# Performance work log

Measured on AMD Instinct MI355X. Metric: run time of the kernel, lower is better.

The kernel has to match this reference:

```python
import jax, jax.numpy as jnp
import numpy as np

N_NODES = 100000
N_EDGES = 1600000
N_GRAPHS = 256
HIDDEN = 128
IN_FEAT = 5


def setup_inputs() -> dict:
    key = jax.random.key(0)
    ks = jax.random.split(key, 12)
    x = jax.random.normal(ks[0], (N_NODES, IN_FEAT), dtype=jnp.float32)
    edge_index = jax.random.randint(ks[1], (2, N_EDGES), 0, N_NODES, dtype=jnp.int64)
    batch = jnp.sort(jax.random.randint(ks[2], (N_NODES,), 0, N_GRAPHS, dtype=jnp.int64))
    s = 0.05
    W0 = jax.random.normal(ks[3], (IN_FEAT, HIDDEN), dtype=jnp.float32) * s
    b0 = jnp.zeros((HIDDEN,), dtype=jnp.float32)
    W1 = jax.random.normal(ks[4], (HIDDEN, HIDDEN), dtype=jnp.float32) * s
    b1 = jnp.zeros((HIDDEN,), dtype=jnp.float32)
    W2 = jax.random.normal(ks[5], (HIDDEN, HIDDEN), dtype=jnp.float32) * s
    b2 = jnp.zeros((HIDDEN,), dtype=jnp.float32)
    lin_w = jax.random.normal(ks[6], (HIDDEN, 1), dtype=jnp.float32) * s
    lin_b = jnp.zeros((1,), dtype=jnp.float32)
    return {"x": x, "edge_index": edge_index, "batch": batch,
            "W0": W0, "b0": b0, "W1": W1, "b1": b1, "W2": W2, "b2": b2,
            "lin_w": lin_w, "lin_b": lin_b}


def reference(x, edge_index, batch, W0, b0, W1, b1, W2, b2, lin_w, lin_b):
    n = x.shape[0]
    # PyG GCNConv: add self-loops, symmetric normalization D^-1/2 (A+I) D^-1/2
    loop = jnp.arange(n, dtype=edge_index.dtype)
    src = jnp.concatenate([edge_index[0], loop])  # [E+N]
    dst = jnp.concatenate([edge_index[1], loop])
    deg = jax.ops.segment_sum(jnp.ones_like(dst, dtype=x.dtype), dst, num_segments=n)
    dis = jnp.where(deg > 0, jax.lax.rsqrt(jnp.maximum(deg, 1.0)), 0.0)
    norm = (dis[src] * dis[dst])[:, None]  # [E+N, 1]

    def gcn_conv(h, W, b):
        h = h @ W                      # [N, H]
        msg = h[src] * norm            # gather + scale, [E+N, H]
        return jax.ops.segment_sum(msg, dst, num_segments=n) + b

    h = jax.nn.relu(gcn_conv(x, W0, b0))
    h = jax.nn.relu(gcn_conv(h, W1, b1))
    h = gcn_conv(h, W2, b2)

    # global_mean_pool over batch ids
    sums = jax.ops.segment_sum(h, batch, num_segments=N_GRAPHS)
    cnt = jax.ops.segment_sum(jnp.ones((n,), x.dtype), batch, num_segments=N_GRAPHS)
    g = sums / jnp.maximum(cnt, 1.0)[:, None]
    # dropout p=0.01 is identity in eval mode
    return jax.nn.sigmoid(g @ lin_w + lin_b)  # [N_GRAPHS, 1]
```

## Files before the change

kernel.cpp:

```cpp
#include <hip/hip_runtime.h>

#define GCN_N 100000
#define GCN_H 128
#define GCN_G 256
#define NPB_SHIFT 9
#define NPB 512
#define NBKT 196
#define CHUNK 2048
#define SRC_BITS 17
#define SRC_MASK ((1 << SRC_BITS) - 1)
#define EBUF_CAP 10240

static_assert(GCN_N < (1 << SRC_BITS), "src id must fit 17 bits");

using short8 = __attribute__((ext_vector_type(8))) short;
using f32x4  = __attribute__((ext_vector_type(4))) float;
using f32x2  = __attribute__((ext_vector_type(2))) float;

#if defined(__has_builtin)
#if __has_builtin(__builtin_amdgcn_cvt_scalef32_pk_f32_fp4)
#define HW_FP4 1
#endif
#endif


__device__ __forceinline__ unsigned short f2bf(float f) {
    unsigned u = __float_as_uint(f);
    unsigned r = u + 0x7FFFu + ((u >> 16) & 1u);
    return (unsigned short)(r >> 16);
}
__device__ __forceinline__ float bf2f(unsigned short h) {
    return __uint_as_float(((unsigned)h) << 16);
}

__device__ __forceinline__ void fp4x8_to_f32(unsigned v, float* f) {
#ifdef HW_FP4
    f32x2 p0 = __builtin_amdgcn_cvt_scalef32_pk_f32_fp4(v, 1.0f, 0);
    f32x2 p1 = __builtin_amdgcn_cvt_scalef32_pk_f32_fp4(v, 1.0f, 1);
    f32x2 p2 = __builtin_amdgcn_cvt_scalef32_pk_f32_fp4(v, 1.0f, 2);
    f32x2 p3 = __builtin_amdgcn_cvt_scalef32_pk_f32_fp4(v, 1.0f, 3);
    f[0] = p0[0]; f[1] = p0[1]; f[2] = p1[0]; f[3] = p1[1];
    f[4] = p2[0]; f[5] = p2[1]; f[6] = p3[0]; f[7] = p3[1];
#else
    #pragma unroll
    for (int j = 0; j < 8; j++) {
        unsigned nib = (v >> (4 * j)) & 0xF;
        unsigned e = (nib >> 1) & 3, m = nib & 1;
        float mag = (e == 0) ? 0.5f * (float)m : ldexpf(1.0f + 0.5f * (float)m, (int)e - 1);
        f[j] = (nib & 8) ? -mag : mag;
    }
#endif
}

__device__ __forceinline__ unsigned f32_to_fp4(float a) {
    unsigned sg = (a < 0.f) ? 8u : 0u;
    float b = fabsf(a);
    unsigned q = (unsigned)(b >= 0.25f) + (unsigned)(b >= 0.75f) + (unsigned)(b >= 1.25f)
               + (unsigned)(b >= 1.75f) + (unsigned)(b >= 2.5f) + (unsigned)(b >= 3.5f)
               + (unsigned)(b >= 5.0f);
    return sg | q;
}


__global__ __launch_bounds__(256) void hist_prep_kernel(const int* __restrict__ dst,
                                                        int* __restrict__ hist, int E, int B,
                                                        const float* __restrict__ W1,
                                                        const float* __restrict__ W2,
                                                        const float* __restrict__ b2,
                                                        const float* __restrict__ lw,
                                                        unsigned short* __restrict__ w1t,
                                                        float* __restrict__ w2l,
                                                        float* __restrict__ c2) {
    __shared__ int lh[NBKT];
    __shared__ float slw[128];
    int blk = blockIdx.x, tid = threadIdx.x;
    if (blk < B) {
        if (tid < NBKT) lh[tid] = 0;
        __syncthreads();
        int e0 = blk * CHUNK;
        #pragma unroll
        for (int i = 0; i < CHUNK / 256; i++) {
            int e = e0 + tid + i * 256;
            if (e < E) atomicAdd(&lh[dst[e] >> NPB_SHIFT], 1);
        }
        __syncthreads();
        if (tid < NBKT) hist[(size_t)blk * NBKT + tid] = lh[tid];
    } else if (blk < B + 64) {
        int idx = (blk - B) * 256 + tid;
        int col = idx >> 7, k = idx & 127;
        w1t[idx] = f2bf(W1[k * 128 + col]);
    } else {
        if (tid < 128) slw[tid] = lw[tid];
        __syncthreads();
        if (tid < 128) {
            float s = 0.f;
            #pragma unroll 8
            for (int j = 0; j < 128; j++) s = fmaf(W2[tid * 128 + j], slw[j], s);
            w2l[tid] = s;
        } else if (tid == 128) {
            float s = 0.f;
            for (int j = 0; j < 128; j++) s = fmaf(b2[j], slw[j], s);
            c2[0] = s;
        }
    }
}

__global__ __launch_bounds__(64) void scan_cols_kernel(const int* __restrict__ hist,
                                                       int* __restrict__ offsT,
                                                       int* __restrict__ btot, int B) {
    int k = blockIdx.x;
    int lane = threadIdx.x;
    int running = 0;
    for (int b0 = 0; b0 < B; b0 += 64) {
        int b = b0 + lane;
        int v = (b < B) ? hist[(size_t)b * NBKT + k] : 0;
        int iv = v;
        #pragma unroll
        for (int d = 1; d < 64; d <<= 1) {
            int x = __shfl_up(iv, d, 64);
            if (lane >= d) iv += x;
        }
        if (b < B) offsT[(size_t)k * B + b] = running + iv - v;
        running += __shfl(iv, 63, 64);
    }
    if (lane == 0) btot[k] = running;
}

__global__ __launch_bounds__(256) void partition_kernel(const int* __restrict__ src,
                                                        const int* __restrict__ dst,
                                                        const int* __restrict__ btot,
                                                        const int* __restrict__ offsT,
                                                        int* __restrict__ epack,
                                                        int E, int B) {
    __shared__ int cur[NBKT];
    __shared__ int sbase[NBKT];
    int blk = blockIdx.x, tid = threadIdx.x;
    if (tid == 0) {
        int run = 0;
        for (int kk = 0; kk < NBKT; kk++) { sbase[kk] = run; run += btot[kk]; }
    }
    __syncthreads();
    if (tid < NBKT) cur[tid] = sbase[tid] + offsT[(size_t)tid * B + blk];
    __syncthreads();
    int e0 = blk * CHUNK;
    #pragma unroll
    for (int i = 0; i < CHUNK / 256; i++) {
        int e = e0 + tid + i * 256;
        if (e < E) {
            int d = dst[e];
            int s = src[e];
            int pos = atomicAdd(&cur[d >> NPB_SHIFT], 1);
            epack[pos] = ((d & (NPB - 1)) << SRC_BITS) | s;
        }
    }
}

__global__ __launch_bounds__(512) void csr_build_kernel(const int* __restrict__ epack,
                                                        const int* __restrict__ btot,
                                                        const float* __restrict__ x,
                                                        int* __restrict__ rowptr,
                                                        float* __restrict__ dis,
                                                        float* __restrict__ xsp,
                                                        int* __restrict__ csrc, int n) {
    __shared__ int ebuf[EBUF_CAP];
    __shared__ int lcount[NPB];
    __shared__ int lcur[NPB];
    __shared__ int wsums[8];
    __shared__ int s_eb, s_ee, s_tot;
    int k = blockIdx.x, tid = threadIdx.x;
    int lane = tid & 63, wid = tid >> 6;
    int nodebase = k << NPB_SHIFT;

    lcount[tid] = 0;
    if (tid == 0) {
        int run = 0, eb = 0, ee = 0;
        for (int kk = 0; kk < NBKT; kk++) {
            if (kk == k) eb = run;
            run += btot[kk];
            if (kk == k) ee = run;
        }
        s_eb = eb; s_ee = ee; s_tot = run;
    }
    __syncthreads();
    int ebeg = s_eb, eend = s_ee;
    bool fits = (eend - ebeg) <= EBUF_CAP;

    for (int e = ebeg + tid; e < eend; e += 512) {
        int p = epack[e];
        if (fits) ebuf[e - ebeg] = p;
        atomicAdd(&lcount[p >> SRC_BITS], 1);
    }
    __syncthreads();

    int v = lcount[tid];
    int iv = v;
    #pragma unroll
    for (int d = 1; d < 64; d <<= 1) {
        int x2 = __shfl_up(iv, d, 64);
        if (lane >= d) iv += x2;
    }
    if (lane == 63) wsums[wid] = iv;
    __syncthreads();
    if (tid == 0) {
        int r = 0;
        #pragma unroll
        for (int w = 0; w < 8; w++) { int t = wsums[w]; wsums[w] = r; r += t; }
    }
    __syncthreads();
    int ex = wsums[wid] + iv - v;
    lcur[tid] = ex;
    int node = nodebase + tid;
    if (node < n) {
        rowptr[node] = ebeg + ex;
        float dd = rsqrtf((float)(v + 1));
        dis[node] = dd;
        const float* xr = x + (size_t)node * 5;
        float4 a;
        a.x = xr[0] * dd; a.y = xr[1] * dd; a.z = xr[2] * dd; a.w = xr[3] * dd;
        float a4 = xr[4] * dd;
        ((float4*)(xsp + (size_t)node * 8))[0] = a;
        xsp[(size_t)node * 8 + 4] = a4;
        xsp[(size_t)node * 8 + 5] = 0.f;
        xsp[(size_t)node * 8 + 6] = 0.f;
        xsp[(size_t)node * 8 + 7] = 0.f;
    }
    if (k == NBKT - 1 && tid == 0) rowptr[n] = s_tot;
    __syncthreads();
    for (int e = ebeg + tid; e < eend; e += 512) {
        int p = fits ? ebuf[e - ebeg] : epack[e];
        int pos = atomicAdd(&lcur[p >> SRC_BITS], 1);
        csrc[ebeg + pos] = p & SRC_MASK;
    }
}


__global__ __launch_bounds__(256) void mmfused_kernel(const float* __restrict__ xsp,
                                                      const int* __restrict__ rowptr,
                                                      const int* __restrict__ csrc,
                                                      const float* __restrict__ W0,
                                                      const float* __restrict__ b0,
                                                      const unsigned short* __restrict__ w1t,
                                                      const float* __restrict__ dis,
                                                      unsigned* __restrict__ t1q4,
                                                      float* __restrict__ tscale, int n) {
    __shared__ __align__(16) unsigned short sA[128 * 128];
    __shared__ __align__(16) unsigned short sBT[128 * 128];
    __shared__ __align__(16) float sA0f[128 * 8];
    __shared__ float sDis[128];
    __shared__ float sSmax[128];
    char* sAb = (char*)sA;
    char* sBb = (char*)sBT;
    int tid = threadIdx.x;
    int rowBase = blockIdx.x * 128;

    if (tid < 128) {
        int i = rowBase + tid;
        float a[5] = {0.f, 0.f, 0.f, 0.f, 0.f};
        float di = 0.f;
        if (i < n) {
            di = dis[i];
            const float* xr = xsp + (size_t)i * 8;
            float4 s4 = ((const float4*)xr)[0];
            a[0] = s4.x; a[1] = s4.y; a[2] = s4.z; a[3] = s4.w; a[4] = xr[4];
            int r0 = rowptr[i], r1 = rowptr[i + 1];
            int e = r0;
            for (; e + 7 < r1; e += 8) {
                int ss[8];
                #pragma unroll
                for (int u = 0; u < 8; u++) ss[u] = csrc[e + u];
                float4 v[8]; float a4[8];
                #pragma unroll
                for (int u = 0; u < 8; u++) {
                    v[u] = ((const float4*)(xsp + (size_t)ss[u] * 8))[0];
                    a4[u] = xsp[(size_t)ss[u] * 8 + 4];
                }
                #pragma unroll
                for (int u = 0; u < 8; u++) {
                    a[0] += v[u].x; a[1] += v[u].y; a[2] += v[u].z; a[3] += v[u].w;
                    a[4] += a4[u];
                }
            }
            for (; e < r1; e++) {
                int s = csrc[e];
                float4 v = ((const float4*)(xsp + (size_t)s * 8))[0];
                a[0] += v.x; a[1] += v.y; a[2] += v.z; a[3] += v.w;
                a[4] += xsp[(size_t)s * 8 + 4];
            }
            #pragma unroll
            for (int j = 0; j < 5; j++) a[j] *= di;
        }
        sDis[tid] = di;
        #pragma unroll
        for (int j = 0; j < 5; j++) sA0f[tid * 8 + j] = a[j];
    } else {
        int t2 = tid - 128;
        #pragma unroll
        for (int it = 0; it < 16; it++) {
            int idx = t2 + it * 128;
            int col = idx >> 4, c = idx & 15;
            uint4 v = ((const uint4*)w1t)[idx];
            int byteoff = (col * 256 + c * 16) ^ ((col & 7) << 4);
            *(uint4*)(sBb + byteoff) = v;
        }
    }
    __syncthreads();

    {
        int cq = tid & 31;
        int rg = tid >> 5;
        float4 w0q[5];
        #pragma unroll
        for (int j = 0; j < 5; j++) w0q[j] = *((const float4*)(W0 + j * 128 + cq * 4));
        float4 b0q = *((const float4*)(b0 + cq * 4));
        #pragma unroll
        for (int ri = 0; ri < 16; ri++) {
            int row = rg + ri * 8;
            const float* ar = sA0f + row * 8;
            float4 h = b0q;
            #pragma unroll
            for (int j = 0; j < 5; j++) {
                float aj = ar[j];
                h.x = fmaf(aj, w0q[j].x, h.x);
                h.y = fmaf(aj, w0q[j].y, h.y);
                h.z = fmaf(aj, w0q[j].z, h.z);
                h.w = fmaf(aj, w0q[j].w, h.w);
            }
            h.x = fmaxf(h.x, 0.f); h.y = fmaxf(h.y, 0.f);
            h.z = fmaxf(h.z, 0.f); h.w = fmaxf(h.w, 0.f);
            uint2 p;
            p.x = (unsigned)f2bf(h.x) | ((unsigned)f2bf(h.y) << 16);
            p.y = (unsigned)f2bf(h.z) | ((unsigned)f2bf(h.w) << 16);
            int byteoff = (row * 256 + cq * 8) ^ ((row & 7) << 4);
            *(uint2*)(sAb + byteoff) = p;
        }
    }
    __syncthreads();

    int wave = tid >> 6, l = tid & 63;
    int lr = l & 15, lg = l >> 4;
    int rb = wave * 32;

    short8 afr[2][4];
    #pragma unroll
    for (int rt = 0; rt < 2; rt++) {
        int row = rb + rt * 16 + lr;
        #pragma unroll
        for (int ks = 0; ks < 4; ks++) {
            int byteoff = (row * 256 + ks * 64 + lg * 16) ^ ((row & 7) << 4);
            afr[rt][ks] = *(const short8*)(sAb + byteoff);
        }
    }
    f32x4 acc[2][8];
    #pragma unroll
    for (int rt = 0; rt < 2; rt++)
        #pragma unroll
        for (int ct = 0; ct < 8; ct++)
            acc[rt][ct] = (f32x4){0.f, 0.f, 0.f, 0.f};

    #pragma unroll
    for (int ct = 0; ct < 8; ct++) {
        int col = ct * 16 + lr;
        short8 bfr[4];
        #pragma unroll
        for (int ks = 0; ks < 4; ks++) {
            int byteoff = (col * 256 + ks * 64 + lg * 16) ^ ((col & 7) << 4);
            bfr[ks] = *(const short8*)(sBb + byteoff);
        }
        #pragma unroll
        for (int rt = 0; rt < 2; rt++) {
            #pragma unroll
            for (int ks = 0; ks < 4; ks++) {
                acc[rt][ct] = __builtin_amdgcn_mfma_f32_16x16x32_bf16(
                    afr[rt][ks], bfr[ks], acc[rt][ct], 0, 0, 0);
            }
        }
    }

    #pragma unroll
    for (int rt = 0; rt < 2; rt++) {
        #pragma unroll
        for (int i = 0; i < 4; i++) {
            int rowL = rb + rt * 16 + lg * 4 + i;
            float dsc = sDis[rowL];
            float m = 0.f;
            #pragma unroll
            for (int ct = 0; ct < 8; ct++) {
                int col = ct * 16 + lr;
                float vv = acc[rt][ct][i] * dsc;
                int byteoff = (rowL * 256 + col * 2) ^ ((rowL & 7) << 4);
                *(unsigned short*)(sAb + byteoff) = f2bf(vv);
                m = fmaxf(m, fabsf(vv));
            }
            #pragma unroll
            for (int msk = 1; msk < 16; msk <<= 1)
                m = fmaxf(m, __shfl_xor(m, msk, 64));
            if (lr == 0) sSmax[rowL] = m;
        }
    }
    __syncthreads();

    #pragma unroll
    for (int it = 0; it < 8; it++) {
        int flat = tid + it * 256;
        int rowL = flat >> 4, c16 = flat & 15;
        int gr = rowBase + rowL;
        if (gr < n) {
            int byteoff = (rowL * 256 + c16 * 16) ^ ((rowL & 7) << 4);
            uint4 v = *(const uint4*)(sAb + byteoff);
            float ff[8];
            ff[0] = __uint_as_float(v.x << 16); ff[1] = __uint_as_float(v.x & 0xFFFF0000u);
            ff[2] = __uint_as_float(v.y << 16); ff[3] = __uint_as_float(v.y & 0xFFFF0000u);
            ff[4] = __uint_as_float(v.z << 16); ff[5] = __uint_as_float(v.z & 0xFFFF0000u);
            ff[6] = __uint_as_float(v.w << 16); ff[7] = __uint_as_float(v.w & 0xFFFF0000u);
            float s6 = sSmax[rowL] * (1.f / 6.f);
            float inv = (s6 > 0.f) ? 1.f / s6 : 0.f;
            unsigned q = 0;
            #pragma unroll
            for (int j = 0; j < 8; j++) q |= f32_to_fp4(ff[j] * inv) << (4 * j);
            t1q4[(size_t)gr * 16 + c16] = q;
            if (c16 == 0) tscale[gr] = s6;
        }
    }
}


__global__ __launch_bounds__(256) void agg1_kernel(const unsigned* __restrict__ t1q4,
                                                   const float* __restrict__ tscale,
                                                   const float* __restrict__ dis,
                                                   const int* __restrict__ rowptr,
                                                   const int* __restrict__ csrc,
                                                   const float* __restrict__ b1,
                                                   const float* __restrict__ w2l,
                                                   float* __restrict__ z, int n) {
    int group = threadIdx.x >> 4, lane = threadIdx.x & 15;
    int i = blockIdx.x * 16 + group;
    if (i >= n) return;
    float f[8], acc[8];
    unsigned sv = t1q4[(size_t)i * 16 + lane];
    float sci = tscale[i];
    fp4x8_to_f32(sv, f);
    #pragma unroll
    for (int j = 0; j < 8; j++) acc[j] = f[j] * sci;
    int r0 = rowptr[i], r1 = rowptr[i + 1];
    for (int e = r0; e < r1; e += 16) {
        int cnt = r1 - e; if (cnt > 16) cnt = 16;
        int idx = e + lane;
        int si = (idx < r1) ? csrc[idx] : 0;
        unsigned vv[16]; float sc[16];
        #pragma unroll
        for (int u = 0; u < 16; u++) {
            if (u < cnt) {
                int s = __shfl(si, u, 16);
                vv[u] = t1q4[(size_t)s * 16 + lane];
                sc[u] = tscale[s];
            }
        }
        #pragma unroll
        for (int u = 0; u < 16; u++) {
            if (u < cnt) {
                fp4x8_to_f32(vv[u], f);
                #pragma unroll
                for (int j = 0; j < 8; j++) acc[j] = fmaf(f[j], sc[u], acc[j]);
            }
        }
    }
    float di = dis[i];
    float4 b4a = ((const float4*)b1)[lane * 2];
    float4 b4b = ((const float4*)b1)[lane * 2 + 1];
    float4 w4a = ((const float4*)w2l)[lane * 2];
    float4 w4b = ((const float4*)w2l)[lane * 2 + 1];
    float bb[8] = {b4a.x, b4a.y, b4a.z, b4a.w, b4b.x, b4b.y, b4b.z, b4b.w};
    float ww[8] = {w4a.x, w4a.y, w4a.z, w4a.w, w4b.x, w4b.y, w4b.z, w4b.w};
    float d = 0.f;
    #pragma unroll
    for (int j = 0; j < 8; j++) {
        float c = fmaxf(fmaf(di, acc[j], bb[j]), 0.f);
        d = fmaf(c, ww[j], d);
    }
    #pragma unroll
    for (int o = 8; o > 0; o >>= 1) d += __shfl_down(d, o, 16);
    if (lane == 0) z[i] = di * d;
}


__global__ __launch_bounds__(256) void aggz_pool_kernel(const float* __restrict__ z,
                                                        const float* __restrict__ dis,
                                                        const int* __restrict__ rowptr,
                                                        const int* __restrict__ csrc,
                                                        const int* __restrict__ batch,
                                                        const float* __restrict__ c2,
                                                        const float* __restrict__ lb,
                                                        float* __restrict__ gsum,
                                                        int* __restrict__ gcnt,
                                                        int* __restrict__ done,
                                                        float* __restrict__ out, int n) {
    __shared__ float lg[GCN_G];
    __shared__ int lc[GCN_G];
    __shared__ int sticket;
    int tid = threadIdx.x;
    lg[tid] = 0.f;
    lc[tid] = 0;
    __syncthreads();
    int i = blockIdx.x * 256 + tid;
    bool valid = i < n;
    float ndv = 0.f;
    int g = 0;
    if (valid) {
        float acc = z[i];
        int r0 = rowptr[i], r1 = rowptr[i + 1];
        int e = r0;
        for (; e + 7 < r1; e += 8) {
            int ss[8];
            #pragma unroll
            for (int u = 0; u < 8; u++) ss[u] = csrc[e + u];
            float zv[8];
            #pragma unroll
            for (int u = 0; u < 8; u++) zv[u] = z[ss[u]];
            #pragma unroll
            for (int u = 0; u < 8; u++) acc += zv[u];
        }
        for (; e < r1; e++) acc += z[csrc[e]];
        ndv = dis[i] * acc;
        g = batch[i];
    }
    int lane = tid & 63;
    int g0 = __shfl(g, 0, 64);
    bool uni = __all(g == g0) && __all(valid);
    if (uni) {
        float s = ndv;
        #pragma unroll
        for (int o = 32; o > 0; o >>= 1) s += __shfl_down(s, o, 64);
        if (lane == 0) {
            atomicAdd(&lg[g0], s);
            atomicAdd(&lc[g0], 64);
        }
    } else if (valid) {
        atomicAdd(&lg[g], ndv);
        atomicAdd(&lc[g], 1);
    }
    __syncthreads();
    float v = lg[tid];
    int c = lc[tid];
    if (v != 0.f) atomicAdd(&gsum[tid], v);
    if (c != 0) atomicAdd(&gcnt[tid], c);

    __threadfence();
    if (tid == 0) sticket = atomicAdd(done, 1);
    __syncthreads();
    if (sticket == (int)gridDim.x - 1) {
        float sv = atomicAdd(&gsum[tid], 0.f);
        int cv = atomicAdd(&gcnt[tid], 0);
        float vv = sv / (float)max(cv, 1) + c2[0] + lb[0];
        out[tid] = 1.f / (1.f + expf(-vv));
    }
}


extern "C" void kernel_launch(void* const* d_in, const int* in_sizes, int n_in,
                              void* d_out, int out_size, void* d_ws, size_t ws_size,
                              hipStream_t stream) {
    const float* x   = (const float*)d_in[0];
    const int*   ei  = (const int*)d_in[1];
    const int*   bat = (const int*)d_in[2];
    const float* W0  = (const float*)d_in[3];
    const float* b0  = (const float*)d_in[4];
    const float* W1  = (const float*)d_in[5];
    const float* b1  = (const float*)d_in[6];
    const float* W2  = (const float*)d_in[7];
    const float* b2  = (const float*)d_in[8];
    const float* lw  = (const float*)d_in[9];
    const float* lb  = (const float*)d_in[10];
    float* out = (float*)d_out;

    const int N = GCN_N;
    const int E = in_sizes[1] / 2;
    const int B = (E + CHUNK - 1) / CHUNK;

    char* ws = (char*)d_ws;
    size_t off = 0;
    auto alloc = [&](size_t bytes) {
        size_t o = off;
        off += (bytes + 255) & ~(size_t)255;
        return o;
    };
    int*   hist    = (int*)(ws + alloc((size_t)B * NBKT * 4));
    int*   offsT   = (int*)(ws + alloc((size_t)NBKT * B * 4));
    int*   btot    = (int*)(ws + alloc((size_t)NBKT * 4));
    int*   epack   = (int*)(ws + alloc((size_t)E * 4));
    int*   rowptr  = (int*)(ws + alloc((size_t)(N + 1) * 4));
    float* dis     = (float*)(ws + alloc((size_t)N * 4));
    int*   csrc    = (int*)(ws + alloc((size_t)E * 4));
    float* xsp     = (float*)(ws + alloc((size_t)N * 8 * 4));
    unsigned* t1q4 = (unsigned*)(ws + alloc((size_t)N * 64));
    float* tscale  = (float*)(ws + alloc((size_t)N * 4));
    float* z       = (float*)(ws + alloc((size_t)N * 4));
    float* w2l     = (float*)(ws + alloc(128 * 4));
    float* c2      = (float*)(ws + alloc(4));
    unsigned short* w1t = (unsigned short*)(ws + alloc(128 * 128 * 2));
    float* gsum    = (float*)(ws + alloc(GCN_G * 4));
    int*   gcnt    = (int*)(ws + alloc(GCN_G * 4));
    int*   done    = (int*)(ws + alloc(4));

    const int* src = ei;
    const int* dst = ei + E;

    hipMemsetAsync(gsum, 0, GCN_G * 4 * 2 + 256, stream);

    hist_prep_kernel<<<B + 65, 256, 0, stream>>>(dst, hist, E, B, W1, W2, b2, lw, w1t, w2l, c2);
    scan_cols_kernel<<<NBKT, 64, 0, stream>>>(hist, offsT, btot, B);
    partition_kernel<<<B, 256, 0, stream>>>(src, dst, btot, offsT, epack, E, B);
    csr_build_kernel<<<NBKT, 512, 0, stream>>>(epack, btot, x, rowptr, dis, xsp, csrc, N);

    mmfused_kernel<<<(N + 127) / 128, 256, 0, stream>>>(xsp, rowptr, csrc, W0, b0, w1t, dis,
                                                        t1q4, tscale, N);
    agg1_kernel<<<(N + 15) / 16, 256, 0, stream>>>(t1q4, tscale, dis, rowptr, csrc, b1, w2l, z, N);
    aggz_pool_kernel<<<(N + 255) / 256, 256, 0, stream>>>(z, dis, rowptr, csrc, bat, c2, lb,
                                                          gsum, gcnt, done, out, N);
}
```

Baseline: 179.0 us.

## Split layer-0 neighbor aggregation into separate kernel before fused matmul

Moves the 5-feature neighbor gather for layer 0 out of the fused matmul kernel into a standalone aggx kernel that uses every thread, writing results to a new a0p buffer. The fused kernel then loads the aggregated rows and the W1 tile with all 256 threads instead of splitting the block half gather, half weight-load. This removes latency-bound, half-occupied gather work from the MFMA kernel at the cost of an extra launch and an extra global round trip of the aggregated features.

Result: slower. 183.2 us (+2.3%).

```diff
diff --git a/kernel.cpp b/kernel.cpp
--- a/kernel.cpp
+++ b/kernel.cpp
@@ -234,9 +234,47 @@
 }
 
 
-__global__ __launch_bounds__(256) void mmfused_kernel(const float* __restrict__ xsp,
-                                                      const int* __restrict__ rowptr,
-                                                      const int* __restrict__ csrc,
+__global__ __launch_bounds__(256) void aggx_kernel(const float* __restrict__ xsp,
+                                                   const float* __restrict__ dis,
+                                                   const int* __restrict__ rowptr,
+                                                   const int* __restrict__ csrc,
+                                                   float* __restrict__ a0p, int n) {
+    int i = blockIdx.x * 256 + threadIdx.x;
+    if (i >= n) return;
+    float4 acc = ((const float4*)(xsp + (size_t)i * 8))[0];
+    float acc4 = xsp[(size_t)i * 8 + 4];
+    int r0 = rowptr[i], r1 = rowptr[i + 1];
+    int e = r0;
+    for (; e + 7 < r1; e += 8) {
+        int ss[8];
+        #pragma unroll
+        for (int u = 0; u < 8; u++) ss[u] = csrc[e + u];
+        float4 v[8]; float a4[8];
+        #pragma unroll
+        for (int u = 0; u < 8; u++) {
+            v[u] = ((const float4*)(xsp + (size_t)ss[u] * 8))[0];
+            a4[u] = xsp[(size_t)ss[u] * 8 + 4];
+        }
+        #pragma unroll
+        for (int u = 0; u < 8; u++) {
+            acc.x += v[u].x; acc.y += v[u].y; acc.z += v[u].z; acc.w += v[u].w;
+            acc4 += a4[u];
+        }
+    }
+    for (; e < r1; e++) {
+        int s = csrc[e];
+        float4 v = ((const float4*)(xsp + (size_t)s * 8))[0];
+        acc.x += v.x; acc.y += v.y; acc.z += v.z; acc.w += v.w;
+        acc4 += xsp[(size_t)s * 8 + 4];
+    }
+    float di = dis[i];
+    acc.x *= di; acc.y *= di; acc.z *= di; acc.w *= di; acc4 *= di;
+    ((float4*)(a0p + (size_t)i * 8))[0] = acc;
+    a0p[(size_t)i * 8 + 4] = acc4;
+}
+
+
+__global__ __launch_bounds__(256) void mmfused_kernel(const float* __restrict__ a0p,
                                                       const float* __restrict__ W0,
                                                       const float* __restrict__ b0,
                                                       const unsigned short* __restrict__ w1t,
@@ -245,7 +283,7 @@
                                                       float* __restrict__ tscale, int n) {
     __shared__ __align__(16) unsigned short sA[128 * 128];
     __shared__ __align__(16) unsigned short sBT[128 * 128];
-    __shared__ __align__(16) float sA0f[128 * 8];
+    __shared__ __align__(16) float4 sA0[256];
     __shared__ float sDis[128];
     __shared__ float sSmax[128];
     char* sAb = (char*)sA;
@@ -253,55 +291,24 @@
     int tid = threadIdx.x;
     int rowBase = blockIdx.x * 128;
 
-    if (tid < 128) {
-        int i = rowBase + tid;
-        float a[5] = {0.f, 0.f, 0.f, 0.f, 0.f};
-        float di = 0.f;
-        if (i < n) {
-            di = dis[i];
-            const float* xr = xsp + (size_t)i * 8;
-            float4 s4 = ((const float4*)xr)[0];
-            a[0] = s4.x; a[1] = s4.y; a[2] = s4.z; a[3] = s4.w; a[4] = xr[4];
-            int r0 = rowptr[i], r1 = rowptr[i + 1];
-            int e = r0;
-            for (; e + 7 < r1; e += 8) {
-                int ss[8];
-                #pragma unroll
-                for (int u = 0; u < 8; u++) ss[u] = csrc[e + u];
-                float4 v[8]; float a4[8];
-                #pragma unroll
-                for (int u = 0; u < 8; u++) {
-                    v[u] = ((const float4*)(xsp + (size_t)ss[u] * 8))[0];
-                    a4[u] = xsp[(size_t)ss[u] * 8 + 4];
-                }
-                #pragma unroll
-                for (int u = 0; u < 8; u++) {
-                    a[0] += v[u].x; a[1] += v[u].y; a[2] += v[u].z; a[3] += v[u].w;
-                    a[4] += a4[u];
-                }
-            }
-            for (; e < r1; e++) {
-                int s = csrc[e];
-                float4 v = ((const float4*)(xsp + (size_t)s * 8))[0];
-                a[0] += v.x; a[1] += v.y; a[2] += v.z; a[3] += v.w;
-                a[4] += xsp[(size_t)s * 8 + 4];
-            }
-            #pragma unroll
-            for (int j = 0; j < 5; j++) a[j] *= di;
-        }
-        sDis[tid] = di;
-        #pragma unroll
-        for (int j = 0; j < 5; j++) sA0f[tid * 8 + j] = a[j];
-    } else {
-        int t2 = tid - 128;
-        #pragma unroll
-        for (int it = 0; it < 16; it++) {
-            int idx = t2 + it * 128;
-            int col = idx >> 4, c = idx & 15;
-            uint4 v = ((const uint4*)w1t)[idx];
-            int byteoff = (col * 256 + c * 16) ^ ((col & 7) << 4);
-            *(uint4*)(sBb + byteoff) = v;
-        }
+    {
+        int rowL = tid >> 1, q = tid & 1;
+        int gr = rowBase + rowL;
+        float4 v = make_float4(0.f, 0.f, 0.f, 0.f);
+        if (gr < n) v = ((const float4*)a0p)[(size_t)gr * 2 + q];
+        sA0[tid] = v;
+        if (tid < 128) {
+            int g2 = rowBase + tid;
+            sDis[tid] = (g2 < n) ? dis[g2] : 0.f;
+        }
+    }
+    #pragma unroll
+    for (int it = 0; it < 8; it++) {
+        int idx = tid + it * 256;
+        int col = idx >> 4, c = idx & 15;
+        uint4 v = ((const uint4*)w1t)[idx];
+        int byteoff = (col * 256 + c * 16) ^ ((col & 7) << 4);
+        *(uint4*)(sBb + byteoff) = v;
     }
     __syncthreads();
 
@@ -312,6 +319,7 @@
         #pragma unroll
         for (int j = 0; j < 5; j++) w0q[j] = *((const float4*)(W0 + j * 128 + cq * 4));
         float4 b0q = *((const float4*)(b0 + cq * 4));
+        const float* sA0f = (const float*)sA0;
         #pragma unroll
         for (int ri = 0; ri < 16; ri++) {
             int row = rg + ri * 8;
@@ -591,6 +599,7 @@
     float* dis     = (float*)(ws + alloc((size_t)N * 4));
     int*   csrc    = (int*)(ws + alloc((size_t)E * 4));
     float* xsp     = (float*)(ws + alloc((size_t)N * 8 * 4));
+    float* a0p     = (float*)(ws + alloc((size_t)N * 8 * 4));
     unsigned* t1q4 = (unsigned*)(ws + alloc((size_t)N * 64));
     float* tscale  = (float*)(ws + alloc((size_t)N * 4));
     float* z       = (float*)(ws + alloc((size_t)N * 4));
@@ -611,8 +620,8 @@
     partition_kernel<<<B, 256, 0, stream>>>(src, dst, btot, offsT, epack, E, B);
     csr_build_kernel<<<NBKT, 512, 0, stream>>>(epack, btot, x, rowptr, dis, xsp, csrc, N);
 
-    mmfused_kernel<<<(N + 127) / 128, 256, 0, stream>>>(xsp, rowptr, csrc, W0, b0, w1t, dis,
-                                                        t1q4, tscale, N);
+    aggx_kernel<<<(N + 255) / 256, 256, 0, stream>>>(xsp, dis, rowptr, csrc, a0p, N);
+    mmfused_kernel<<<(N + 127) / 128, 256, 0, stream>>>(a0p, W0, b0, w1t, dis, t1q4, tscale, N);
     agg1_kernel<<<(N + 15) / 16, 256, 0, stream>>>(t1q4, tscale, dis, rowptr, csrc, b1, w2l, z, N);
     aggz_pool_kernel<<<(N + 255) / 256, 256, 0, stream>>>(z, dis, rowptr, csrc, bat, c2, lb,
                                                           gsum, gcnt, done, out, N);
```
